# Kernel tuning notes

Measured on AMD Instinct MI355X. Metric: run time of the kernel, lower is better.

The kernel has to match this reference:

```python
import jax, jax.numpy as jnp
from jax import lax
import numpy as np

C_IN, C_OUT, G, K, PAD = 64, 128, 4, 3, 1
P = K * K
CG = C_IN // G
N, H, W = 8, 64, 64
LN_EPS = 1e-6
BN_EPS = 1e-5


def setup_inputs() -> dict:
    key = jax.random.key(0)
    ks = jax.random.split(key, 32)
    r = lambda i, shape, s=0.05: jax.random.normal(ks[i], shape, dtype=jnp.float32) * s
    return dict(
        x=jax.random.normal(ks[0], (N, C_IN, H, W), dtype=jnp.float32),
        reflectance=jax.random.uniform(ks[1], (N, 1, H, W), dtype=jnp.float32),
        gain_w1=r(2, (C_IN, C_IN // 4)), gain_b1=r(3, (C_IN // 4,)),
        gain_w2=r(4, (C_IN // 4, C_IN)), gain_b2=r(5, (C_IN,)),
        tap_w=r(6, (C_IN,)), tap_b=r(7, (C_IN,)),
        dw_w=r(8, (K, K, 1, C_IN)), dw_b=r(9, (C_IN,)),
        ln_g=jnp.ones((C_IN,), jnp.float32), ln_b=jnp.zeros((C_IN,), jnp.float32),
        inp_w=r(10, (C_IN, C_IN)), inp_b=r(11, (C_IN,)),
        off_w=r(12, (C_IN, G * P * 2), 0.02), off_b=r(13, (G * P * 2,), 0.02),
        mask_w=r(14, (C_IN, G * P), 0.02), mask_b=r(15, (G * P,), 0.02),
        outp_w=r(16, (C_IN, C_IN)), outp_b=r(17, (C_IN,)),
        conv_w=r(18, (C_IN, C_OUT)), conv_b=r(19, (C_OUT,)),
        bn1_g=jnp.ones((C_IN,), jnp.float32), bn1_b=jnp.zeros((C_IN,), jnp.float32),
        bn1_m=r(20, (C_IN,)),
        bn1_v=jax.random.uniform(ks[21], (C_IN,), minval=0.5, maxval=1.5),
        bn2_g=jnp.ones((C_OUT,), jnp.float32), bn2_b=jnp.zeros((C_OUT,), jnp.float32),
        bn2_m=r(22, (C_OUT,)),
        bn2_v=jax.random.uniform(ks[23], (C_OUT,), minval=0.5, maxval=1.5),
    )


def _bilinear_gather(xg, py, px):
    # xg: (N, Hp, Wp, G, CG); py/px: (N, H, W, G, P) absolute pixel coords
    # replicates F.grid_sample(mode='bilinear', padding_mode='zeros', align_corners=False)
    n_, Hp, Wp = xg.shape[0], xg.shape[1], xg.shape[2]
    y0 = jnp.floor(py)
    x0 = jnp.floor(px)
    wy = py - y0
    wx = px - x0
    nI = jnp.arange(n_).reshape(n_, 1, 1, 1, 1)
    gI = jnp.arange(G).reshape(1, 1, 1, G, 1)
    out = jnp.zeros(py.shape + (CG,), xg.dtype)
    for dy in (0, 1):
        for dx in (0, 1):
            yi = y0 + dy
            xi = x0 + dx
            w = (wy if dy else 1.0 - wy) * (wx if dx else 1.0 - wx)
            valid = (yi >= 0) & (yi < Hp) & (xi >= 0) & (xi < Wp)
            yc = jnp.clip(yi, 0, Hp - 1).astype(jnp.int32)
            xc = jnp.clip(xi, 0, Wp - 1).astype(jnp.int32)
            v = xg[nI, yc, xc, gI]  # (N, H, W, G, P, CG)
            out = out + (w * valid.astype(w.dtype))[..., None] * v
    return out


def reference(x, reflectance, gain_w1, gain_b1, gain_w2, gain_b2, tap_w, tap_b,
              dw_w, dw_b, ln_g, ln_b, inp_w, inp_b, off_w, off_b, mask_w, mask_b,
              outp_w, outp_b, conv_w, conv_b, bn1_g, bn1_b, bn1_m, bn1_v,
              bn2_g, bn2_b, bn2_m, bn2_v):
    n_, c_, h_, w_ = x.shape
    # ---- GainBlock (SE-style): x * sigmoid(mlp(avgpool(x))) + x ----
    pooled = x.mean(axis=(2, 3))                               # (N, C)
    g = jax.nn.relu(pooled @ gain_w1 + gain_b1)
    gain = jax.nn.sigmoid(g @ gain_w2 + gain_b2)               # (N, C)
    x = x * gain[:, :, None, None] + x
    # ---- ReflectiveFeedback: x + relu(conv1x1(reflectance)) ----
    refl = jax.nn.relu(reflectance * tap_w[None, :, None, None] + tap_b[None, :, None, None])
    x = x + refl                                               # (N, C, H, W)
    # ---- DCNv3 (pytorch version, group=4, k=3, pad=1, stride=1) ----
    xh = jnp.transpose(x, (0, 2, 3, 1))                        # NHWC
    xp = xh @ inp_w + inp_b                                    # input_proj
    dw = lax.conv_general_dilated(xh, dw_w, (1, 1), 'SAME',
                                  feature_group_count=c_,
                                  dimension_numbers=('NHWC', 'HWIO', 'NHWC')) + dw_b
    mu = dw.mean(-1, keepdims=True)
    var = dw.var(-1, keepdims=True)
    dw = ln_g * (dw - mu) * lax.rsqrt(var + LN_EPS) + ln_b     # LN channels_last
    dw = jax.nn.gelu(dw, approximate=False)
    offset = (dw @ off_w + off_b).reshape(n_, h_, w_, G, P, 2)
    mask = jax.nn.softmax((dw @ mask_w + mask_b).reshape(n_, h_, w_, G, P), axis=-1)
    # dcnv3_core: pad input, build reference + dilation grids (normalized by padded size)
    xpad = jnp.pad(xp, ((0, 0), (PAD, PAD), (PAD, PAD), (0, 0)))
    Hp, Wp = h_ + 2 * PAD, w_ + 2 * PAD
    ctr = (K - 1) // 2  # = (dilation*(k-1))//2 with dilation=1
    ref_y = (jnp.arange(h_, dtype=jnp.float32) + ctr + 0.5) / Hp
    ref_x = (jnp.arange(w_, dtype=jnp.float32) + ctr + 0.5) / Wp
    kk = jnp.arange(K, dtype=jnp.float32) - ctr                # [-1, 0, 1]
    gx = jnp.repeat(kk, K) / Wp                                # w-outer, h-inner order
    gy = jnp.tile(kk, K) / Hp
    loc_x = (ref_x[None, None, :, None, None] + gx[None, None, None, None, :]
             + offset[..., 0] / Wp)                            # (N,H,W,G,P)
    loc_y = (ref_y[None, :, None, None, None] + gy[None, None, None, None, :]
             + offset[..., 1] / Hp)
    px = loc_x * Wp - 0.5   # align_corners=False pixel coords
    py = loc_y * Hp - 0.5
    xg = xpad.reshape(n_, Hp, Wp, G, CG)
    samp = _bilinear_gather(xg, py, px)                        # (N,H,W,G,P,CG)
    dcn = (samp * mask[..., None]).sum(axis=4).reshape(n_, h_, w_, c_)
    dcn = dcn @ outp_w + outp_b                                # output_proj
    y = jnp.transpose(dcn, (0, 3, 1, 2))                       # back to NCHW
    # ---- bn1 -> relu -> conv1x1 -> bn2 -> relu (eval-mode BN) ----
    y = bn1_g[None, :, None, None] * (y - bn1_m[None, :, None, None]) \
        * lax.rsqrt(bn1_v[None, :, None, None] + BN_EPS) + bn1_b[None, :, None, None]
    y = jax.nn.relu(y)
    y = jnp.einsum('nchw,cd->ndhw', y, conv_w) + conv_b[None, :, None, None]
    y = bn2_g[None, :, None, None] * (y - bn2_m[None, :, None, None]) \
        * lax.rsqrt(bn2_v[None, :, None, None] + BN_EPS) + bn2_b[None, :, None, None]
    return jax.nn.relu(y)
```

## Files before the change

### kernel.cpp

```cpp
#include <hip/hip_runtime.h>
#include <math.h>


#define WAVE_FENCE() asm volatile("s_waitcnt lgkmcnt(0)" ::: "memory")

__global__ __launch_bounds__(256) void k_pool(const float* x, float* pooled) {
    __shared__ float red[256];
    int b = blockIdx.x;
    int nc = ((b & 7) << 6) | (b >> 3);
    const float4* p4 = reinterpret_cast<const float4*>(x + (size_t)nc * 4096);
    float s = 0.f;
    for (int i = threadIdx.x; i < 1024; i += 256) {
        float4 v = p4[i];
        s += v.x + v.y + v.z + v.w;
    }
    red[threadIdx.x] = s;
    __syncthreads();
    for (int o = 128; o > 0; o >>= 1) {
        if (threadIdx.x < o) red[threadIdx.x] += red[threadIdx.x + o];
        __syncthreads();
    }
    if (threadIdx.x == 0) pooled[nc] = red[0] * (1.f / 4096.f);
}

__global__ __launch_bounds__(64) void k_gain(const float* pooled,
        const float* gw1, const float* gb1,
        const float* gw2, const float* gb2,
        float* gain) {
    int n = blockIdx.x;
    int lane = threadIdx.x;
    float pv = pooled[n * 64 + lane];
    float part[16];
    const float4* g4 = reinterpret_cast<const float4*>(gw1 + lane * 16);
    #pragma unroll
    for (int q = 0; q < 4; ++q) {
        float4 v = g4[q];
        part[q * 4 + 0] = pv * v.x;
        part[q * 4 + 1] = pv * v.y;
        part[q * 4 + 2] = pv * v.z;
        part[q * 4 + 3] = pv * v.w;
    }
    #pragma unroll
    for (int o = 32; o > 0; o >>= 1) {
        #pragma unroll
        for (int j = 0; j < 16; ++j) part[j] += __shfl_xor(part[j], o, 64);
    }
    float acc = gb2[lane];
    #pragma unroll
    for (int j = 0; j < 16; ++j) {
        float hj = fmaxf(part[j] + gb1[j], 0.f);
        acc += hj * gw2[j * 64 + lane];
    }
    gain[n * 64 + lane] = 1.f + 1.f / (1.f + __expf(-acc));
}

__global__ __launch_bounds__(128) void k_xsproj(
        const float* x, const float* refl,
        const float* tap_w, const float* tap_b,
        const float* gain,
        const float* inp_w, const float* inp_b,
        float* xs, float* xpad) {
    __shared__ float xsrow[2][4][64];
    int tid = threadIdx.x;
    int lane = tid & 63, wv = tid >> 6;
    int b = blockIdx.x;
    int n = b & 7, rem = b >> 3;
    int h = rem >> 3, wc = rem & 7;
    int w0 = wc * 8 + wv * 4;
    int nh = n * 64 + h;
    float (*xr)[64] = xsrow[wv];

    {
        float4 xv = *reinterpret_cast<const float4*>(
            &x[(((size_t)(n * 64 + lane)) * 64 + h) * 64 + w0]);
        float gv = gain[n * 64 + lane];
        float tw = tap_w[lane], tb = tap_b[lane];
        const float* rp = refl + n * 4096 + h * 64 + w0;
        float xvv[4] = {xv.x, xv.y, xv.z, xv.w};
        #pragma unroll
        for (int i = 0; i < 4; ++i) {
            float r = fmaxf(rp[i] * tw + tb, 0.f);
            float v = xvv[i] * gv + r;
            xr[i][lane] = v;
            xs[(((size_t)nh) * 64 + w0 + i) * 64 + lane] = v;
        }
    }
    WAVE_FENCE();

    {
        float acc[4];
        float bv = inp_b[lane];
        #pragma unroll
        for (int i = 0; i < 4; ++i) acc[i] = bv;
        #pragma unroll
        for (int c4 = 0; c4 < 64; c4 += 4) {
            float q0 = inp_w[(c4 + 0) * 64 + lane];
            float q1 = inp_w[(c4 + 1) * 64 + lane];
            float q2 = inp_w[(c4 + 2) * 64 + lane];
            float q3 = inp_w[(c4 + 3) * 64 + lane];
            #pragma unroll
            for (int i = 0; i < 4; ++i) {
                float4 d = *reinterpret_cast<const float4*>(&xr[i][c4]);
                acc[i] += d.x * q0 + d.y * q1 + d.z * q2 + d.w * q3;
            }
        }
        const size_t rowb = (((size_t)n * 66) + (h + 1)) * 66;
        #pragma unroll
        for (int i = 0; i < 4; ++i)
            xpad[(rowb + (w0 + i + 1)) * 64 + lane] = acc[i];
        if (w0 == 0)  xpad[rowb * 64 + lane] = 0.f;
        if (w0 == 60) xpad[(rowb + 65) * 64 + lane] = 0.f;
        if (h == 0 || h == 63) {
            const size_t rb = (((size_t)n * 66) + (h == 0 ? 0 : 65)) * 66;
            #pragma unroll
            for (int i = 0; i < 4; ++i)
                xpad[(rb + 1 + w0 + i) * 64 + lane] = 0.f;
            if (w0 == 0)  xpad[rb * 64 + lane] = 0.f;
            if (w0 == 60) xpad[(rb + 65) * 64 + lane] = 0.f;
        }
    }
}

__global__ __launch_bounds__(128, 4) void k_dwsamp(const float* xs, const float* xpad,
                       const float* dw_w, const float* dw_b,
                       const float* ln_g, const float* ln_b,
                       const float* off_w, const float* off_b,
                       const float* mask_w, const float* mask_b,
                       const float* outp_w, const float* outp_b,
                       const float* bn1_g, const float* bn1_b,
                       const float* bn1_m, const float* bn1_v,
                       const float* conv_w, const float* conv_b,
                       const float* bn2_g, const float* bn2_b,
                       const float* bn2_m, const float* bn2_v,
                       float* out) {
    __shared__ float smem[2816];

    int tid = threadIdx.x;
    int lane = tid & 63, wv = tid >> 6;
    float*  chunk = smem + wv * 1408;
    int4*   sad   = reinterpret_cast<int4*>(chunk);
    float*  dwr   = chunk;
    float4* swt   = reinterpret_cast<float4*>(chunk + 576);
    float*  dcnl  = chunk + 1152;
    float*  mlog  = chunk + 1152;

    int b = blockIdx.x;
    int n = b & 7;
    int pos0 = (b >> 3) * 8 + wv * 4;
    int h = pos0 >> 6, w0 = pos0 & 63;

    {
        float dwk[9];
        #pragma unroll
        for (int k = 0; k < 9; ++k) dwk[k] = dw_w[k * 64 + lane];
        float s[4];
        float bvv = dw_b[lane];
        #pragma unroll
        for (int p = 0; p < 4; ++p) s[p] = bvv;
        for (int ky = 0; ky < 3; ++ky) {
            int y = h + ky - 1;
            if (y < 0 || y > 63) continue;
            const float* xrow = xs + ((size_t)(n * 64 + y)) * 4096;
            float v[6];
            #pragma unroll
            for (int dx = 0; dx < 6; ++dx) {
                int x2 = w0 - 1 + dx;
                v[dx] = (x2 >= 0 && x2 <= 63) ? xrow[x2 * 64 + lane] : 0.f;
            }
            float k0 = dwk[ky * 3 + 0], k1 = dwk[ky * 3 + 1], k2 = dwk[ky * 3 + 2];
            #pragma unroll
            for (int p = 0; p < 4; ++p)
                s[p] += v[p] * k0 + v[p + 1] * k1 + v[p + 2] * k2;
        }
        float lngv = ln_g[lane], lnbv = ln_b[lane];
        #pragma unroll
        for (int p = 0; p < 4; ++p) {
            float sv = s[p];
            float sum = sv, sq = sv * sv;
            #pragma unroll
            for (int o = 32; o > 0; o >>= 1) {
                sum += __shfl_xor(sum, o, 64);
                sq  += __shfl_xor(sq,  o, 64);
            }
            float mu = sum * (1.f / 64.f);
            float var = sq * (1.f / 64.f) - mu * mu;
            float nrm = (sv - mu) * rsqrtf(var + 1e-6f) * lngv + lnbv;
            dwr[p * 64 + lane] = 0.5f * nrm * (1.f + erff(nrm * 0.70710678118654752f));
        }
    }
    WAVE_FENCE();

    float a0[4], a1[4];
    {
        int jb = lane * 2;
        const float* wptr;
        int stride;
        float b0 = 0.f, b1 = 0.f;
        if (lane < 36)      { wptr = off_w + jb;         stride = 72; b0 = off_b[jb];       b1 = off_b[jb + 1]; }
        else if (lane < 54) { wptr = mask_w + (jb - 72); stride = 36; b0 = mask_b[jb - 72]; b1 = mask_b[jb - 71]; }
        else                { wptr = off_w;              stride = 0; }
        #pragma unroll
        for (int p = 0; p < 4; ++p) { a0[p] = b0; a1[p] = b1; }
        for (int c4 = 0; c4 < 64; c4 += 4) {
            float4 d0 = *reinterpret_cast<const float4*>(&dwr[0 * 64 + c4]);
            float4 d1 = *reinterpret_cast<const float4*>(&dwr[1 * 64 + c4]);
            float4 d2 = *reinterpret_cast<const float4*>(&dwr[2 * 64 + c4]);
            float4 d3 = *reinterpret_cast<const float4*>(&dwr[3 * 64 + c4]);
            float dk0[4] = {d0.x, d0.y, d0.z, d0.w};
            float dk1[4] = {d1.x, d1.y, d1.z, d1.w};
            float dk2[4] = {d2.x, d2.y, d2.z, d2.w};
            float dk3[4] = {d3.x, d3.y, d3.z, d3.w};
            #pragma unroll
            for (int k = 0; k < 4; ++k) {
                float2 w2 = *reinterpret_cast<const float2*>(wptr);
                wptr += stride;
                a0[0] += dk0[k] * w2.x;  a1[0] += dk0[k] * w2.y;
                a0[1] += dk1[k] * w2.x;  a1[1] += dk1[k] * w2.y;
                a0[2] += dk2[k] * w2.x;  a1[2] += dk2[k] * w2.y;
                a0[3] += dk3[k] * w2.x;  a1[3] += dk3[k] * w2.y;
            }
        }
        if (lane >= 36 && lane < 54) {
            int jm = lane * 2 - 72;
            #pragma unroll
            for (int p = 0; p < 4; ++p) {
                mlog[p * 40 + jm]     = a0[p];
                mlog[p * 40 + jm + 1] = a1[p];
            }
        }
    }
    WAVE_FENCE();

    if (lane < 36) {
        int g = lane / 9, pp = lane - g * 9;
        #pragma unroll
        for (int p = 0; p < 4; ++p) {
            const float* lrow = &mlog[p * 40 + g * 9];
            float m = lrow[0];
            #pragma unroll
            for (int k = 1; k < 9; ++k) m = fmaxf(m, lrow[k]);
            float ssum = 0.f, ek = 0.f;
            #pragma unroll
            for (int k = 0; k < 9; ++k) {
                float e = __expf(lrow[k] - m);
                ssum += e;
                if (k == pp) ek = e;
            }
            float mk = ek / ssum;
            float px = (float)((w0 + p) + (pp / 3)) + a0[p];
            float py = (float)(h + (pp % 3)) + a1[p];
            float x0f = floorf(px), y0f = floorf(py);
            float wx = px - x0f, wy = py - y0f;
            int x0 = (int)x0f, y0 = (int)y0f;
            int x1 = x0 + 1, y1 = y0 + 1;
            int xc0 = min(max(x0, 0), 65), xc1 = min(max(x1, 0), 65);
            int yc0 = min(max(y0, 0), 65), yc1 = min(max(y1, 0), 65);
            float vx0 = (x0 >= 0 && x0 < 66) ? 1.f : 0.f;
            float vx1 = (x1 >= 0 && x1 < 66) ? 1.f : 0.f;
            float vy0 = (y0 >= 0 && y0 < 66) ? 1.f : 0.f;
            float vy1 = (y1 >= 0 && y1 < 66) ? 1.f : 0.f;
            float wx0 = (1.f - wx) * vx0, wx1 = wx * vx1;
            float wy0 = (1.f - wy) * vy0, wy1 = wy * vy1;
            swt[p * 36 + lane] = make_float4(mk * wy0 * wx0, mk * wy0 * wx1,
                                             mk * wy1 * wx0, mk * wy1 * wx1);
            sad[p * 36 + lane] = make_int4((yc0 * 66 + xc0) * 64, (yc0 * 66 + xc1) * 64,
                                           (yc1 * 66 + xc0) * 64, (yc1 * 66 + xc1) * 64);
        }
    }
    WAVE_FENCE();

    {
        int gb = (lane >> 4) * 9;
        const float* xpn = xpad + (size_t)n * 66 * 66 * 64;
        #pragma unroll
        for (int p = 0; p < 4; ++p) {
            float t0[9], t1[9], t2[9], t3[9];
            #pragma unroll
            for (int pp = 0; pp < 9; ++pp) {
                int4 a = sad[p * 36 + gb + pp];
                t0[pp] = xpn[a.x + lane];
                t1[pp] = xpn[a.y + lane];
                t2[pp] = xpn[a.z + lane];
                t3[pp] = xpn[a.w + lane];
            }
            float acc = 0.f;
            #pragma unroll
            for (int pp = 0; pp < 9; ++pp) {
                float4 cw = swt[p * 36 + gb + pp];
                acc += cw.x * t0[pp] + cw.y * t1[pp]
                     + cw.z * t2[pp] + cw.w * t3[pp];
            }
            dcnl[p * 64 + lane] = acc;
        }
    }
    WAVE_FENCE();

    {
        float ob = outp_b[lane];
        float s0 = ob, s1 = ob, s2 = ob, s3 = ob;
        for (int c4 = 0; c4 < 64; c4 += 4) {
            float w0v = outp_w[(c4 + 0) * 64 + lane];
            float w1v = outp_w[(c4 + 1) * 64 + lane];
            float w2v = outp_w[(c4 + 2) * 64 + lane];
            float w3v = outp_w[(c4 + 3) * 64 + lane];
            float4 d0 = *reinterpret_cast<const float4*>(&dcnl[0 * 64 + c4]);
            float4 d1 = *reinterpret_cast<const float4*>(&dcnl[1 * 64 + c4]);
            float4 d2 = *reinterpret_cast<const float4*>(&dcnl[2 * 64 + c4]);
            float4 d3 = *reinterpret_cast<const float4*>(&dcnl[3 * 64 + c4]);
            s0 += d0.x * w0v + d0.y * w1v + d0.z * w2v + d0.w * w3v;
            s1 += d1.x * w0v + d1.y * w1v + d1.z * w2v + d1.w * w3v;
            s2 += d2.x * w0v + d2.y * w1v + d2.z * w2v + d2.w * w3v;
            s3 += d3.x * w0v + d3.y * w1v + d3.z * w2v + d3.w * w3v;
        }
        float sc = bn1_g[lane] * rsqrtf(bn1_v[lane] + 1e-5f);
        float sh = bn1_b[lane] - sc * bn1_m[lane];
        WAVE_FENCE();
        dcnl[0 * 64 + lane] = fmaxf(sc * s0 + sh, 0.f);
        dcnl[1 * 64 + lane] = fmaxf(sc * s1 + sh, 0.f);
        dcnl[2 * 64 + lane] = fmaxf(sc * s2 + sh, 0.f);
        dcnl[3 * 64 + lane] = fmaxf(sc * s3 + sh, 0.f);
    }
    WAVE_FENCE();

    {
        float accA[4], accB[4];
        #pragma unroll
        for (int p = 0; p < 4; ++p) { accA[p] = 0.f; accB[p] = 0.f; }
        for (int c4 = 0; c4 < 64; c4 += 4) {
            float4 d0 = *reinterpret_cast<const float4*>(&dcnl[0 * 64 + c4]);
            float4 d1 = *reinterpret_cast<const float4*>(&dcnl[1 * 64 + c4]);
            float4 d2 = *reinterpret_cast<const float4*>(&dcnl[2 * 64 + c4]);
            float4 d3 = *reinterpret_cast<const float4*>(&dcnl[3 * 64 + c4]);
            float dk0[4] = {d0.x, d0.y, d0.z, d0.w};
            float dk1[4] = {d1.x, d1.y, d1.z, d1.w};
            float dk2[4] = {d2.x, d2.y, d2.z, d2.w};
            float dk3[4] = {d3.x, d3.y, d3.z, d3.w};
            #pragma unroll
            for (int k = 0; k < 4; ++k) {
                float wa = conv_w[(c4 + k) * 128 + lane];
                float wb = conv_w[(c4 + k) * 128 + 64 + lane];
                accA[0] += dk0[k] * wa;  accB[0] += dk0[k] * wb;
                accA[1] += dk1[k] * wa;  accB[1] += dk1[k] * wb;
                accA[2] += dk2[k] * wa;  accB[2] += dk2[k] * wb;
                accA[3] += dk3[k] * wa;  accB[3] += dk3[k] * wb;
            }
        }
        int dA = lane, dB = lane + 64;
        float scA = bn2_g[dA] * rsqrtf(bn2_v[dA] + 1e-5f);
        float shA = scA * (conv_b[dA] - bn2_m[dA]) + bn2_b[dA];
        float scB = bn2_g[dB] * rsqrtf(bn2_v[dB] + 1e-5f);
        float shB = scB * (conv_b[dB] - bn2_m[dB]) + bn2_b[dB];
        float4 rA, rB;
        rA.x = fmaxf(scA * accA[0] + shA, 0.f);
        rA.y = fmaxf(scA * accA[1] + shA, 0.f);
        rA.z = fmaxf(scA * accA[2] + shA, 0.f);
        rA.w = fmaxf(scA * accA[3] + shA, 0.f);
        rB.x = fmaxf(scB * accB[0] + shB, 0.f);
        rB.y = fmaxf(scB * accB[1] + shB, 0.f);
        rB.z = fmaxf(scB * accB[2] + shB, 0.f);
        rB.w = fmaxf(scB * accB[3] + shB, 0.f);
        size_t oA = (((size_t)(n * 128 + dA)) * 64 + h) * 64 + w0;
        size_t oB = (((size_t)(n * 128 + dB)) * 64 + h) * 64 + w0;
        *reinterpret_cast<float4*>(out + oA) = rA;
        *reinterpret_cast<float4*>(out + oB) = rB;
    }
}

extern "C" void kernel_launch(void* const* d_in, const int* in_sizes, int n_in,
                              void* d_out, int out_size, void* d_ws, size_t ws_size,
                              hipStream_t stream) {
    const float* x      = (const float*)d_in[0];
    const float* refl   = (const float*)d_in[1];
    const float* gw1    = (const float*)d_in[2];
    const float* gb1    = (const float*)d_in[3];
    const float* gw2    = (const float*)d_in[4];
    const float* gb2    = (const float*)d_in[5];
    const float* tap_w  = (const float*)d_in[6];
    const float* tap_b  = (const float*)d_in[7];
    const float* dw_w   = (const float*)d_in[8];
    const float* dw_b   = (const float*)d_in[9];
    const float* ln_g   = (const float*)d_in[10];
    const float* ln_b   = (const float*)d_in[11];
    const float* inp_w  = (const float*)d_in[12];
    const float* inp_b  = (const float*)d_in[13];
    const float* off_w  = (const float*)d_in[14];
    const float* off_b  = (const float*)d_in[15];
    const float* mask_w = (const float*)d_in[16];
    const float* mask_b = (const float*)d_in[17];
    const float* outp_w = (const float*)d_in[18];
    const float* outp_b = (const float*)d_in[19];
    const float* conv_w = (const float*)d_in[20];
    const float* conv_b = (const float*)d_in[21];
    const float* bn1_g  = (const float*)d_in[22];
    const float* bn1_b  = (const float*)d_in[23];
    const float* bn1_m  = (const float*)d_in[24];
    const float* bn1_v  = (const float*)d_in[25];
    const float* bn2_g  = (const float*)d_in[26];
    const float* bn2_b  = (const float*)d_in[27];
    const float* bn2_m  = (const float*)d_in[28];
    const float* bn2_v  = (const float*)d_in[29];

    float* ws     = (float*)d_ws;
    float* pooled = ws;
    float* gaing  = ws + 512;
    float* xs     = ws + 1024;
    float* xpad   = xs + 2097152;

    k_pool<<<512, 256, 0, stream>>>(x, pooled);
    k_gain<<<8, 64, 0, stream>>>(pooled, gw1, gb1, gw2, gb2, gaing);
    k_xsproj<<<4096, 128, 0, stream>>>(x, refl, tap_w, tap_b, gaing,
                                       inp_w, inp_b, xs, xpad);
    k_dwsamp<<<4096, 128, 0, stream>>>(xs, xpad, dw_w, dw_b, ln_g, ln_b,
                                       off_w, off_b, mask_w, mask_b,
                                       outp_w, outp_b, bn1_g, bn1_b, bn1_m, bn1_v,
                                       conv_w, conv_b, bn2_g, bn2_b, bn2_m, bn2_v,
                                       (float*)d_out);
}
```

Baseline: 193.5 us.

## Process a full image row per block in xsproj via shared-memory transpose tile

The xs/input-projection kernel now handles a whole (n,h) row of 64 pixels per 256-thread block instead of 8 pixels per 128-thread block. It loads the NCHW row coalesced with float4 into a padded shared tile, transposes it to NHWC in shared memory, and amortizes the inp_w loads over 16 pixels per thread. The aim is to fix the poorly coalesced strided x reads and reduce redundant weight traffic, at the cost of only 512 blocks, fewer waves in flight and more registers per thread.

```diff
diff --git a/kernel.cpp b/kernel.cpp
--- a/kernel.cpp
+++ b/kernel.cpp
@@ -54,69 +54,76 @@
     gain[n * 64 + lane] = 1.f + 1.f / (1.f + __expf(-acc));
 }
 
-__global__ __launch_bounds__(128) void k_xsproj(
+__global__ __launch_bounds__(256) void k_xsproj(
         const float* x, const float* refl,
         const float* tap_w, const float* tap_b,
         const float* gain,
         const float* inp_w, const float* inp_b,
         float* xs, float* xpad) {
-    __shared__ float xsrow[2][4][64];
-    int tid = threadIdx.x;
-    int lane = tid & 63, wv = tid >> 6;
+    __shared__ float tile[64][65];
+    __shared__ float xsw[64][68];
+    __shared__ float rr[64];
+    int t = threadIdx.x;
     int b = blockIdx.x;
-    int n = b & 7, rem = b >> 3;
-    int h = rem >> 3, wc = rem & 7;
-    int w0 = wc * 8 + wv * 4;
-    int nh = n * 64 + h;
-    float (*xr)[64] = xsrow[wv];
-
-    {
-        float4 xv = *reinterpret_cast<const float4*>(
-            &x[(((size_t)(n * 64 + lane)) * 64 + h) * 64 + w0]);
-        float gv = gain[n * 64 + lane];
-        float tw = tap_w[lane], tb = tap_b[lane];
-        const float* rp = refl + n * 4096 + h * 64 + w0;
-        float xvv[4] = {xv.x, xv.y, xv.z, xv.w};
-        #pragma unroll
-        for (int i = 0; i < 4; ++i) {
-            float r = fmaxf(rp[i] * tw + tb, 0.f);
-            float v = xvv[i] * gv + r;
-            xr[i][lane] = v;
-            xs[(((size_t)nh) * 64 + w0 + i) * 64 + lane] = v;
-        }
-    }
-    WAVE_FENCE();
-
-    {
-        float acc[4];
-        float bv = inp_b[lane];
-        #pragma unroll
-        for (int i = 0; i < 4; ++i) acc[i] = bv;
-        #pragma unroll
+    int n = b & 7, h = b >> 3;
+    int c = t & 63, g = t >> 6;
+
+    #pragma unroll
+    for (int it = 0; it < 4; ++it) {
+        int f = it * 256 + t;
+        int cc = f >> 4, w4 = (f & 15) * 4;
+        float4 v = *reinterpret_cast<const float4*>(
+            &x[(((size_t)(n * 64 + cc)) * 64 + h) * 64 + w4]);
+        tile[cc][w4 + 0] = v.x;
+        tile[cc][w4 + 1] = v.y;
+        tile[cc][w4 + 2] = v.z;
+        tile[cc][w4 + 3] = v.w;
+    }
+    if (t < 64) rr[t] = refl[n * 4096 + h * 64 + t];
+    __syncthreads();
+
+    {
+        float gv = gain[n * 64 + c];
+        float tw = tap_w[c], tb = tap_b[c];
+        float* xsg = xs + (((size_t)(n * 64 + h)) * 64) * 64 + c;
+        #pragma unroll
+        for (int k = 0; k < 16; ++k) {
+            int w = g * 16 + k;
+            float r = fmaxf(rr[w] * tw + tb, 0.f);
+            float v = tile[c][w] * gv + r;
+            xsw[w][c] = v;
+            xsg[(size_t)w * 64] = v;
+        }
+    }
+    __syncthreads();
+
+    {
+        float acc[16];
+        float bv = inp_b[c];
+        #pragma unroll
+        for (int k = 0; k < 16; ++k) acc[k] = bv;
         for (int c4 = 0; c4 < 64; c4 += 4) {
-            float q0 = inp_w[(c4 + 0) * 64 + lane];
-            float q1 = inp_w[(c4 + 1) * 64 + lane];
-            float q2 = inp_w[(c4 + 2) * 64 + lane];
-            float q3 = inp_w[(c4 + 3) * 64 + lane];
-            #pragma unroll
-            for (int i = 0; i < 4; ++i) {
-                float4 d = *reinterpret_cast<const float4*>(&xr[i][c4]);
-                acc[i] += d.x * q0 + d.y * q1 + d.z * q2 + d.w * q3;
+            float q0 = inp_w[(c4 + 0) * 64 + c];
+            float q1 = inp_w[(c4 + 1) * 64 + c];
+            float q2 = inp_w[(c4 + 2) * 64 + c];
+            float q3 = inp_w[(c4 + 3) * 64 + c];
+            #pragma unroll
+            for (int k = 0; k < 16; ++k) {
+                float4 d = *reinterpret_cast<const float4*>(&xsw[g * 16 + k][c4]);
+                acc[k] += d.x * q0 + d.y * q1 + d.z * q2 + d.w * q3;
             }
         }
         const size_t rowb = (((size_t)n * 66) + (h + 1)) * 66;
         #pragma unroll
-        for (int i = 0; i < 4; ++i)
-            xpad[(rowb + (w0 + i + 1)) * 64 + lane] = acc[i];
-        if (w0 == 0)  xpad[rowb * 64 + lane] = 0.f;
-        if (w0 == 60) xpad[(rowb + 65) * 64 + lane] = 0.f;
+        for (int k = 0; k < 16; ++k) {
+            int w = g * 16 + k;
+            xpad[(rowb + (w + 1)) * 64 + c] = acc[k];
+        }
+        if (g == 0) xpad[rowb * 64 + c] = 0.f;
+        if (g == 3) xpad[(rowb + 65) * 64 + c] = 0.f;
         if (h == 0 || h == 63) {
-            const size_t rb = (((size_t)n * 66) + (h == 0 ? 0 : 65)) * 66;
-            #pragma unroll
-            for (int i = 0; i < 4; ++i)
-                xpad[(rb + 1 + w0 + i) * 64 + lane] = 0.f;
-            if (w0 == 0)  xpad[rb * 64 + lane] = 0.f;
-            if (w0 == 60) xpad[(rb + 65) * 64 + lane] = 0.f;
+            const size_t base = ((((size_t)n * 66) + (h == 0 ? 0 : 65)) * 66) * 64;
+            for (int i = t; i < 66 * 64; i += 256) xpad[base + i] = 0.f;
         }
     }
 }
@@ -408,8 +415,8 @@
 
     k_pool<<<512, 256, 0, stream>>>(x, pooled);
     k_gain<<<8, 64, 0, stream>>>(pooled, gw1, gb1, gw2, gb2, gaing);
-    k_xsproj<<<4096, 128, 0, stream>>>(x, refl, tap_w, tap_b, gaing,
-                                       inp_w, inp_b, xs, xpad);
+    k_xsproj<<<512, 256, 0, stream>>>(x, refl, tap_w, tap_b, gaing,
+                                      inp_w, inp_b, xs, xpad);
     k_dwsamp<<<4096, 128, 0, stream>>>(xs, xpad, dw_w, dw_b, ln_g, ln_b,
                                        off_w, off_b, mask_w, mask_b,
                                        outp_w, outp_b, bn1_g, bn1_b, bn1_m, bn1_v,
```

New measurement: 197.9 us. +2.3%, slower.
